# Optimization experiments

Hardware: AMD Instinct MI355X
Metric: run time of the kernel (lower is better)

## Reference

```python
import jax, jax.numpy as jnp
import numpy as np

HIDDEN = 128
INPUT_SIZE = 64
NUM_ACTIONS = 16
BATCH = 65536


def _uniform(key, shape, scale):
    return jax.random.uniform(key, shape, jnp.float32, -scale, scale)


def setup_inputs() -> dict:
    key = jax.random.key(0)
    ks = jax.random.split(key, 14)
    s = 1.0 / np.sqrt(HIDDEN)  # pytorch LSTM/Linear init scale
    return {
        "x": jax.random.normal(ks[0], (BATCH, INPUT_SIZE), jnp.float32),
        # layer 0 LSTM weights (gate order: i, f, g, o)
        "Wih0": _uniform(ks[1], (4 * HIDDEN, INPUT_SIZE), s),
        "Whh0": _uniform(ks[2], (4 * HIDDEN, HIDDEN), s),
        "bih0": _uniform(ks[3], (4 * HIDDEN,), s),
        "bhh0": _uniform(ks[4], (4 * HIDDEN,), s),
        # layer 1 LSTM weights
        "Wih1": _uniform(ks[5], (4 * HIDDEN, HIDDEN), s),
        "Whh1": _uniform(ks[6], (4 * HIDDEN, HIDDEN), s),
        "bih1": _uniform(ks[7], (4 * HIDDEN,), s),
        "bhh1": _uniform(ks[8], (4 * HIDDEN,), s),
        # policy / value heads
        "Wp": _uniform(ks[9], (NUM_ACTIONS, HIDDEN), s),
        "bp": _uniform(ks[10], (NUM_ACTIONS,), s),
        "Wv": _uniform(ks[11], (1, HIDDEN), s),
        "bv": _uniform(ks[12], (1,), s),
    }


def _lstm_cell(x, h, c, Wih, Whh, bih, bhh):
    # gates: [B, 4H], pytorch gate order i, f, g, o
    g = x @ Wih.T + bih + h @ Whh.T + bhh
    i, f, gg, o = jnp.split(g, 4, axis=-1)
    i = jax.nn.sigmoid(i)
    f = jax.nn.sigmoid(f)
    gg = jnp.tanh(gg)
    o = jax.nn.sigmoid(o)
    c2 = f * c + i * gg
    h2 = o * jnp.tanh(c2)
    return h2, c2


def reference(x, Wih0, Whh0, bih0, bhh0, Wih1, Whh1, bih1, bhh1, Wp, bp, Wv, bv):
    B = x.shape[0]
    z = jnp.zeros((B, HIDDEN), x.dtype)  # state=None -> zero init
    # seq_len == 1: single step through the 2-layer stack
    h0, c0 = _lstm_cell(x, z, z, Wih0, Whh0, bih0, bhh0)
    h1, c1 = _lstm_cell(h0, z, z, Wih1, Whh1, bih1, bhh1)
    out = h1[None]  # [1, B, H] like pytorch LSTM output
    policy = out @ Wp.T + bp  # gumbel=True -> raw logits
    value = out @ Wv.T + bv
    return policy, value
```

## Files before the change

### kernel.cpp

```cpp
#include <hip/hip_runtime.h>
#include <hip/hip_bf16.h>

#define BATCH 65536
#define IN    64
#define H     128
#define NA    16
#define NBLK  256
#define TPB   512

typedef __bf16 bf16x8 __attribute__((ext_vector_type(8)));
typedef float  f32x4  __attribute__((ext_vector_type(4)));

union Frag { uint4 u; bf16x8 v; };
struct F32x8 { float4 a, b; };

#define EXP2F(v) __builtin_amdgcn_exp2f(v)
#define RCPF(v)  __builtin_amdgcn_rcpf(v)
#define K1 1.442695041f
#define K2 2.885390082f

__device__ __forceinline__ F32x8 ld8f(const float* p) {
    F32x8 r;
    r.a = *reinterpret_cast<const float4*>(p);
    r.b = *reinterpret_cast<const float4*>(p + 4);
    return r;
}
__device__ __forceinline__ Frag cvt8(F32x8 x) {
    Frag f;
    f.v[0]=(__bf16)x.a.x; f.v[1]=(__bf16)x.a.y; f.v[2]=(__bf16)x.a.z; f.v[3]=(__bf16)x.a.w;
    f.v[4]=(__bf16)x.b.x; f.v[5]=(__bf16)x.b.y; f.v[6]=(__bf16)x.b.z; f.v[7]=(__bf16)x.b.w;
    return f;
}
__device__ __forceinline__ Frag cvt44(float4 a, float4 b) {
    Frag f;
    f.v[0]=(__bf16)a.x; f.v[1]=(__bf16)a.y; f.v[2]=(__bf16)a.z; f.v[3]=(__bf16)a.w;
    f.v[4]=(__bf16)b.x; f.v[5]=(__bf16)b.y; f.v[6]=(__bf16)b.z; f.v[7]=(__bf16)b.w;
    return f;
}
__device__ __forceinline__ unsigned pk2(float lo, float hi) {
    unsigned short l = __builtin_bit_cast(unsigned short, (__bf16)lo);
    unsigned short h = __builtin_bit_cast(unsigned short, (__bf16)hi);
    return (unsigned)l | ((unsigned)h << 16);
}
__device__ __forceinline__ float clamp30(float v) {
    return __builtin_fminf(__builtin_fmaxf(v, -30.0f), 30.0f);
}
__device__ __forceinline__ float lstm_h(float ip, float gp, float op) {
    ip = clamp30(ip); gp = clamp30(gp); op = clamp30(op);
    const float Ei = EXP2F(-K1 * ip);
    const float Eg = EXP2F( K2 * gp);
    const float c2 = (Eg - 1.0f) * RCPF((1.0f + Ei) * (Eg + 1.0f));
    const float Eo = EXP2F(-K1 * op);
    const float Ec = EXP2F( K2 * c2);
    return (Ec - 1.0f) * RCPF((1.0f + Eo) * (Ec + 1.0f));
}

__global__ __launch_bounds__(TPB, 2)
void lstm_fused(const float* __restrict__ x,
                const float* __restrict__ Wih0,
                const float* __restrict__ bih0,
                const float* __restrict__ bhh0,
                const float* __restrict__ Wih1,
                const float* __restrict__ bih1,
                const float* __restrict__ bhh1,
                const float* __restrict__ Wp,
                const float* __restrict__ bp,
                const float* __restrict__ Wv,
                const float* __restrict__ bv,
                float* __restrict__ out)
{
    __shared__ __align__(16) uint4 w0s[384 * 8];
    __shared__ __align__(16) uint4 w1s[384 * 16];
    __shared__ __align__(16) uint4 wph[32 * 16];
    __shared__ float b0s[384];
    __shared__ float b1s[384];

    const int tid  = threadIdx.x;
    const int wave = tid >> 6;
    const int lane = tid & 63;
    const int q    = lane >> 4;
    const int m    = lane & 15;
    const int rbase = blockIdx.x * 256 + wave * 32;
    const f32x4 vzero = {0.f, 0.f, 0.f, 0.f};

    F32x8 xr[2][2];
#pragma unroll
    for (int s2 = 0; s2 < 2; ++s2) {
        const float* xp = x + (size_t)(rbase + s2 * 16 + m) * IN + q * 8;
        xr[s2][0] = ld8f(xp);
        xr[s2][1] = ld8f(xp + 32);
    }
    const float4 bpr = *reinterpret_cast<const float4*>(bp + q * 4);
    const float  bvv = bv[0];

#pragma unroll
    for (int r = 0; r < 6; ++r) {
        const int idx = tid + (r << 9);
        const int j = idx >> 3, s = idx & 7;
        const int g = j >> 7, h = j & 127;
        const int srow = h + ((g == 0) ? 0 : (g + 1) * 128);
        Frag f = cvt8(ld8f(Wih0 + (size_t)srow * IN + s * 8));
        w0s[(j << 3) + (s ^ (j & 7))] = f.u;
    }
#pragma unroll
    for (int r = 0; r < 12; ++r) {
        const int idx = tid + (r << 9);
        const int j = idx >> 4, s = idx & 15;
        const int g = j >> 7, h = j & 127;
        const int srow = h + ((g == 0) ? 0 : (g + 1) * 128);
        const int kt = s >> 2, qq = s & 3;
        const float* pA = Wih1 + (size_t)srow * H + kt * 32 + qq * 4;
        Frag f = cvt44(*reinterpret_cast<const float4*>(pA),
                       *reinterpret_cast<const float4*>(pA + 16));
        w1s[(j << 4) + (s ^ (j & 7))] = f.u;
    }
    {
        const int j = tid >> 4, s = tid & 15;
        const int kt = s >> 2, qq = s & 3;
        Frag f;
        if (j <= 16) {
            const float* base = (j < 16) ? (Wp + (size_t)j * H) : Wv;
            const float* pA = base + kt * 32 + qq * 4;
            f = cvt44(*reinterpret_cast<const float4*>(pA),
                      *reinterpret_cast<const float4*>(pA + 16));
        } else {
            f.u = make_uint4(0u, 0u, 0u, 0u);
        }
        wph[(j << 4) + (s ^ (j & 7))] = f.u;
    }
#pragma unroll
    for (int r = 0; r < 2; ++r) {
        const int t = tid + (r << 9);
        if (t < 384) {
            const int g = t >> 7, h = t & 127;
            const int srow = h + ((g == 0) ? 0 : (g + 1) * 128);
            b0s[t] = bih0[srow] + bhh0[srow];
        } else if (t < 768) {
            const int tt = t - 384;
            const int g = tt >> 7, h = tt & 127;
            const int srow = h + ((g == 0) ? 0 : (g + 1) * 128);
            b1s[tt] = bih1[srow] + bhh1[srow];
        }
    }

    __syncthreads();

    const int swz = m & 7;
    Frag xb[2][2];
#pragma unroll
    for (int s2 = 0; s2 < 2; ++s2) {
        xb[s2][0] = cvt8(xr[s2][0]);
        xb[s2][1] = cvt8(xr[s2][1]);
    }

    unsigned hw0[2][16];
#pragma unroll
    for (int nc = 0; nc < 8; ++nc) {
        f32x4 acc[3][2];
#pragma unroll
        for (int g = 0; g < 3; ++g) { acc[g][0] = vzero; acc[g][1] = vzero; }
#pragma unroll
        for (int g = 0; g < 3; ++g) {
            const int n = g * 128 + nc * 16 + m;
#pragma unroll
            for (int kt = 0; kt < 2; ++kt) {
                Frag a; a.u = w0s[(n << 3) + ((kt * 4 + q) ^ swz)];
#pragma unroll
                for (int s2 = 0; s2 < 2; ++s2)
                    acc[g][s2] = __builtin_amdgcn_mfma_f32_16x16x32_bf16(
                        a.v, xb[s2][kt].v, acc[g][s2], 0, 0, 0);
            }
        }
        const f32x4 bI = *reinterpret_cast<const f32x4*>(b0s +       nc * 16 + q * 4);
        const f32x4 bG = *reinterpret_cast<const f32x4*>(b0s + 128 + nc * 16 + q * 4);
        const f32x4 bO = *reinterpret_cast<const f32x4*>(b0s + 256 + nc * 16 + q * 4);
#pragma unroll
        for (int s2 = 0; s2 < 2; ++s2)
#pragma unroll
            for (int u = 0; u < 2; ++u) {
                const float ha = lstm_h(acc[0][s2][2*u]   + bI[2*u],
                                        acc[1][s2][2*u]   + bG[2*u],
                                        acc[2][s2][2*u]   + bO[2*u]);
                const float hb = lstm_h(acc[0][s2][2*u+1] + bI[2*u+1],
                                        acc[1][s2][2*u+1] + bG[2*u+1],
                                        acc[2][s2][2*u+1] + bO[2*u+1]);
                hw0[s2][nc * 2 + u] = pk2(ha, hb);
            }
    }

    unsigned hw1[2][16];
#pragma unroll
    for (int nc = 0; nc < 8; ++nc) {
        f32x4 acc[3][2];
#pragma unroll
        for (int g = 0; g < 3; ++g) { acc[g][0] = vzero; acc[g][1] = vzero; }
#pragma unroll
        for (int kt = 0; kt < 4; ++kt) {
            Frag b[2];
#pragma unroll
            for (int s2 = 0; s2 < 2; ++s2)
                b[s2].u = make_uint4(hw0[s2][4*kt], hw0[s2][4*kt+1],
                                     hw0[s2][4*kt+2], hw0[s2][4*kt+3]);
#pragma unroll
            for (int g = 0; g < 3; ++g) {
                const int n = g * 128 + nc * 16 + m;
                Frag a; a.u = w1s[(n << 4) + ((kt * 4 + q) ^ swz)];
#pragma unroll
                for (int s2 = 0; s2 < 2; ++s2)
                    acc[g][s2] = __builtin_amdgcn_mfma_f32_16x16x32_bf16(
                        a.v, b[s2].v, acc[g][s2], 0, 0, 0);
            }
        }
        const f32x4 bI = *reinterpret_cast<const f32x4*>(b1s +       nc * 16 + q * 4);
        const f32x4 bG = *reinterpret_cast<const f32x4*>(b1s + 128 + nc * 16 + q * 4);
        const f32x4 bO = *reinterpret_cast<const f32x4*>(b1s + 256 + nc * 16 + q * 4);
#pragma unroll
        for (int s2 = 0; s2 < 2; ++s2)
#pragma unroll
            for (int u = 0; u < 2; ++u) {
                const float ha = lstm_h(acc[0][s2][2*u]   + bI[2*u],
                                        acc[1][s2][2*u]   + bG[2*u],
                                        acc[2][s2][2*u]   + bO[2*u]);
                const float hb = lstm_h(acc[0][s2][2*u+1] + bI[2*u+1],
                                        acc[1][s2][2*u+1] + bG[2*u+1],
                                        acc[2][s2][2*u+1] + bO[2*u+1]);
                hw1[s2][nc * 2 + u] = pk2(ha, hb);
            }
    }

    f32x4 ap[2], av[2];
    ap[0] = vzero; ap[1] = vzero; av[0] = vzero; av[1] = vzero;
#pragma unroll
    for (int kt = 0; kt < 4; ++kt) {
        Frag a0; a0.u = wph[( m       << 4) + ((kt * 4 + q) ^ swz)];
        Frag a1; a1.u = wph[((16 + m) << 4) + ((kt * 4 + q) ^ swz)];
#pragma unroll
        for (int s2 = 0; s2 < 2; ++s2) {
            Frag b; b.u = make_uint4(hw1[s2][4*kt], hw1[s2][4*kt+1],
                                     hw1[s2][4*kt+2], hw1[s2][4*kt+3]);
            ap[s2] = __builtin_amdgcn_mfma_f32_16x16x32_bf16(a0.v, b.v, ap[s2], 0, 0, 0);
            av[s2] = __builtin_amdgcn_mfma_f32_16x16x32_bf16(a1.v, b.v, av[s2], 0, 0, 0);
        }
    }
#pragma unroll
    for (int s2 = 0; s2 < 2; ++s2) {
        const int row = rbase + s2 * 16 + m;
        f32x4 po;
        po[0] = ap[s2][0] + bpr.x; po[1] = ap[s2][1] + bpr.y;
        po[2] = ap[s2][2] + bpr.z; po[3] = ap[s2][3] + bpr.w;
        *reinterpret_cast<f32x4*>(out + (size_t)row * NA + q * 4) = po;
        if (q == 0) out[(size_t)BATCH * NA + row] = av[s2][0] + bvv;
    }
}

extern "C" void kernel_launch(void* const* d_in, const int* in_sizes, int n_in,
                              void* d_out, int out_size, void* d_ws, size_t ws_size,
                              hipStream_t stream) {
    lstm_fused<<<dim3(NBLK), dim3(TPB), 0, stream>>>(
        (const float*)d_in[0], (const float*)d_in[1],
        (const float*)d_in[3], (const float*)d_in[4],
        (const float*)d_in[5], (const float*)d_in[7],
        (const float*)d_in[8], (const float*)d_in[9],
        (const float*)d_in[10], (const float*)d_in[11],
        (const float*)d_in[12], (float*)d_out);
}
```

Baseline: 107.3 us.

## Fuse head MFMAs into layer-1 loop and keep h0 as fragments

Stores layer-0 hidden outputs directly as packed bf16 MFMA B-fragments instead of a flat word array. It also folds the policy/value head MFMAs into the layer-1 output loop, consuming each pair of column chunks as soon as it is produced, so the full hw1 array is never held. The layer-1 loop is no longer unrolled (unroll 1). The aim is lower register pressure and better MFMA/activation interleaving, at the cost of loop overhead and less scheduling freedom across iterations.

```diff
diff --git a/kernel.cpp b/kernel.cpp
--- a/kernel.cpp
+++ b/kernel.cpp
@@ -153,7 +153,7 @@
         xb[s2][1] = cvt8(xr[s2][1]);
     }
 
-    unsigned hw0[2][16];
+    Frag b1[2][4];
 #pragma unroll
     for (int nc = 0; nc < 8; ++nc) {
         f32x4 acc[3][2];
@@ -175,73 +175,62 @@
         const f32x4 bG = *reinterpret_cast<const f32x4*>(b0s + 128 + nc * 16 + q * 4);
         const f32x4 bO = *reinterpret_cast<const f32x4*>(b0s + 256 + nc * 16 + q * 4);
 #pragma unroll
-        for (int s2 = 0; s2 < 2; ++s2)
-#pragma unroll
-            for (int u = 0; u < 2; ++u) {
-                const float ha = lstm_h(acc[0][s2][2*u]   + bI[2*u],
-                                        acc[1][s2][2*u]   + bG[2*u],
-                                        acc[2][s2][2*u]   + bO[2*u]);
-                const float hb = lstm_h(acc[0][s2][2*u+1] + bI[2*u+1],
-                                        acc[1][s2][2*u+1] + bG[2*u+1],
-                                        acc[2][s2][2*u+1] + bO[2*u+1]);
-                hw0[s2][nc * 2 + u] = pk2(ha, hb);
-            }
-    }
-
-    unsigned hw1[2][16];
-#pragma unroll
+        for (int s2 = 0; s2 < 2; ++s2) {
+            const float h0a = lstm_h(acc[0][s2][0] + bI[0], acc[1][s2][0] + bG[0], acc[2][s2][0] + bO[0]);
+            const float h0b = lstm_h(acc[0][s2][1] + bI[1], acc[1][s2][1] + bG[1], acc[2][s2][1] + bO[1]);
+            const float h1a = lstm_h(acc[0][s2][2] + bI[2], acc[1][s2][2] + bG[2], acc[2][s2][2] + bO[2]);
+            const float h1b = lstm_h(acc[0][s2][3] + bI[3], acc[1][s2][3] + bG[3], acc[2][s2][3] + bO[3]);
+            const unsigned wu0 = pk2(h0a, h0b);
+            const unsigned wu1 = pk2(h1a, h1b);
+            if ((nc & 1) == 0) { b1[s2][nc >> 1].u.x = wu0; b1[s2][nc >> 1].u.y = wu1; }
+            else               { b1[s2][nc >> 1].u.z = wu0; b1[s2][nc >> 1].u.w = wu1; }
+        }
+    }
+
+    f32x4 ap[2], av[2];
+    ap[0] = vzero; ap[1] = vzero; av[0] = vzero; av[1] = vzero;
+    uint2 hold[2];
+#pragma unroll 1
     for (int nc = 0; nc < 8; ++nc) {
         f32x4 acc[3][2];
 #pragma unroll
         for (int g = 0; g < 3; ++g) { acc[g][0] = vzero; acc[g][1] = vzero; }
+        const int nbase = nc * 16 + m;
 #pragma unroll
         for (int kt = 0; kt < 4; ++kt) {
-            Frag b[2];
-#pragma unroll
-            for (int s2 = 0; s2 < 2; ++s2)
-                b[s2].u = make_uint4(hw0[s2][4*kt], hw0[s2][4*kt+1],
-                                     hw0[s2][4*kt+2], hw0[s2][4*kt+3]);
 #pragma unroll
             for (int g = 0; g < 3; ++g) {
-                const int n = g * 128 + nc * 16 + m;
-                Frag a; a.u = w1s[(n << 4) + ((kt * 4 + q) ^ swz)];
+                Frag a; a.u = w1s[((g * 128 + nbase) << 4) + ((kt * 4 + q) ^ swz)];
 #pragma unroll
                 for (int s2 = 0; s2 < 2; ++s2)
                     acc[g][s2] = __builtin_amdgcn_mfma_f32_16x16x32_bf16(
-                        a.v, b[s2].v, acc[g][s2], 0, 0, 0);
+                        a.v, b1[s2][kt].v, acc[g][s2], 0, 0, 0);
             }
         }
         const f32x4 bI = *reinterpret_cast<const f32x4*>(b1s +       nc * 16 + q * 4);
         const f32x4 bG = *reinterpret_cast<const f32x4*>(b1s + 128 + nc * 16 + q * 4);
         const f32x4 bO = *reinterpret_cast<const f32x4*>(b1s + 256 + nc * 16 + q * 4);
 #pragma unroll
-        for (int s2 = 0; s2 < 2; ++s2)
-#pragma unroll
-            for (int u = 0; u < 2; ++u) {
-                const float ha = lstm_h(acc[0][s2][2*u]   + bI[2*u],
-                                        acc[1][s2][2*u]   + bG[2*u],
-                                        acc[2][s2][2*u]   + bO[2*u]);
-                const float hb = lstm_h(acc[0][s2][2*u+1] + bI[2*u+1],
-                                        acc[1][s2][2*u+1] + bG[2*u+1],
-                                        acc[2][s2][2*u+1] + bO[2*u+1]);
-                hw1[s2][nc * 2 + u] = pk2(ha, hb);
+        for (int s2 = 0; s2 < 2; ++s2) {
+            const float h0a = lstm_h(acc[0][s2][0] + bI[0], acc[1][s2][0] + bG[0], acc[2][s2][0] + bO[0]);
+            const float h0b = lstm_h(acc[0][s2][1] + bI[1], acc[1][s2][1] + bG[1], acc[2][s2][1] + bO[1]);
+            const float h1a = lstm_h(acc[0][s2][2] + bI[2], acc[1][s2][2] + bG[2], acc[2][s2][2] + bO[2]);
+            const float h1b = lstm_h(acc[0][s2][3] + bI[3], acc[1][s2][3] + bG[3], acc[2][s2][3] + bO[3]);
+            const unsigned wu0 = pk2(h0a, h0b);
+            const unsigned wu1 = pk2(h1a, h1b);
+            if ((nc & 1) == 0) {
+                hold[s2].x = wu0; hold[s2].y = wu1;
+            } else {
+                Frag bh; bh.u = make_uint4(hold[s2].x, hold[s2].y, wu0, wu1);
+                const int ktp = nc >> 1;
+                Frag a0; a0.u = wph[( m       << 4) + ((ktp * 4 + q) ^ swz)];
+                Frag a1; a1.u = wph[((16 + m) << 4) + ((ktp * 4 + q) ^ swz)];
+                ap[s2] = __builtin_amdgcn_mfma_f32_16x16x32_bf16(a0.v, bh.v, ap[s2], 0, 0, 0);
+                av[s2] = __builtin_amdgcn_mfma_f32_16x16x32_bf16(a1.v, bh.v, av[s2], 0, 0, 0);
             }
-    }
-
-    f32x4 ap[2], av[2];
-    ap[0] = vzero; ap[1] = vzero; av[0] = vzero; av[1] = vzero;
-#pragma unroll
-    for (int kt = 0; kt < 4; ++kt) {
-        Frag a0; a0.u = wph[( m       << 4) + ((kt * 4 + q) ^ swz)];
-        Frag a1; a1.u = wph[((16 + m) << 4) + ((kt * 4 + q) ^ swz)];
-#pragma unroll
-        for (int s2 = 0; s2 < 2; ++s2) {
-            Frag b; b.u = make_uint4(hw1[s2][4*kt], hw1[s2][4*kt+1],
-                                     hw1[s2][4*kt+2], hw1[s2][4*kt+3]);
-            ap[s2] = __builtin_amdgcn_mfma_f32_16x16x32_bf16(a0.v, b.v, ap[s2], 0, 0, 0);
-            av[s2] = __builtin_amdgcn_mfma_f32_16x16x32_bf16(a1.v, b.v, av[s2], 0, 0, 0);
-        }
-    }
+        }
+    }
+
 #pragma unroll
     for (int s2 = 0; s2 < 2; ++s2) {
         const int row = rbase + s2 * 16 + m;
```

Measured after the change: 109.8 us. +2.4%, slower.

## Precompute bf16 swizzled weights and biases in a prep kernel

Applied to the files above, without the earlier changes.

Moves the fp32-to-bf16 conversion, gate reordering, swizzling and bias summation of all weights out of the main kernel into a small prep kernel that writes a packed image to workspace. Each main-kernel block then copies that image into shared memory with plain 16-byte loads, instead of redoing the conversion in all 256 blocks. This adds a second kernel launch and a global round trip through workspace. The per-block weight load also becomes half the bytes.

```diff
diff --git a/kernel.cpp b/kernel.cpp
--- a/kernel.cpp
+++ b/kernel.cpp
@@ -7,6 +7,14 @@
 #define NA    16
 #define NBLK  256
 #define TPB   512
+
+#define NW0   3072
+#define NW1   6144
+#define NPH   512
+#define OW1   3072
+#define OPH   9216
+#define OBIAS 9728
+#define NTOT  9920
 
 typedef __bf16 bf16x8 __attribute__((ext_vector_type(8)));
 typedef float  f32x4  __attribute__((ext_vector_type(4)));
@@ -55,67 +63,40 @@
     return (Ec - 1.0f) * RCPF((1.0f + Eo) * (Ec + 1.0f));
 }
 
-__global__ __launch_bounds__(TPB, 2)
-void lstm_fused(const float* __restrict__ x,
-                const float* __restrict__ Wih0,
-                const float* __restrict__ bih0,
-                const float* __restrict__ bhh0,
-                const float* __restrict__ Wih1,
-                const float* __restrict__ bih1,
-                const float* __restrict__ bhh1,
-                const float* __restrict__ Wp,
-                const float* __restrict__ bp,
-                const float* __restrict__ Wv,
-                const float* __restrict__ bv,
-                float* __restrict__ out)
+__device__ __forceinline__ int igo_row(int j) {
+    const int g = j >> 7, h = j & 127;
+    return h + ((g == 0) ? 0 : (g + 1) * 128);
+}
+
+__global__ __launch_bounds__(256)
+void lstm_prep(const float* __restrict__ Wih0,
+               const float* __restrict__ bih0,
+               const float* __restrict__ bhh0,
+               const float* __restrict__ Wih1,
+               const float* __restrict__ bih1,
+               const float* __restrict__ bhh1,
+               const float* __restrict__ Wp,
+               const float* __restrict__ Wv,
+               uint4* __restrict__ ws)
 {
-    __shared__ __align__(16) uint4 w0s[384 * 8];
-    __shared__ __align__(16) uint4 w1s[384 * 16];
-    __shared__ __align__(16) uint4 wph[32 * 16];
-    __shared__ float b0s[384];
-    __shared__ float b1s[384];
-
-    const int tid  = threadIdx.x;
-    const int wave = tid >> 6;
-    const int lane = tid & 63;
-    const int q    = lane >> 4;
-    const int m    = lane & 15;
-    const int rbase = blockIdx.x * 256 + wave * 32;
-    const f32x4 vzero = {0.f, 0.f, 0.f, 0.f};
-
-    F32x8 xr[2][2];
-#pragma unroll
-    for (int s2 = 0; s2 < 2; ++s2) {
-        const float* xp = x + (size_t)(rbase + s2 * 16 + m) * IN + q * 8;
-        xr[s2][0] = ld8f(xp);
-        xr[s2][1] = ld8f(xp + 32);
-    }
-    const float4 bpr = *reinterpret_cast<const float4*>(bp + q * 4);
-    const float  bvv = bv[0];
-
-#pragma unroll
-    for (int r = 0; r < 6; ++r) {
-        const int idx = tid + (r << 9);
-        const int j = idx >> 3, s = idx & 7;
-        const int g = j >> 7, h = j & 127;
-        const int srow = h + ((g == 0) ? 0 : (g + 1) * 128);
+    const int G = blockIdx.x * 256 + threadIdx.x;
+    if (G < NW0) {
+        const int j = G >> 3, s = G & 7;
+        const int srow = igo_row(j);
         Frag f = cvt8(ld8f(Wih0 + (size_t)srow * IN + s * 8));
-        w0s[(j << 3) + (s ^ (j & 7))] = f.u;
-    }
-#pragma unroll
-    for (int r = 0; r < 12; ++r) {
-        const int idx = tid + (r << 9);
-        const int j = idx >> 4, s = idx & 15;
-        const int g = j >> 7, h = j & 127;
-        const int srow = h + ((g == 0) ? 0 : (g + 1) * 128);
+        ws[(j << 3) + (s ^ (j & 7))] = f.u;
+    } else if (G < OPH) {
+        const int t = G - OW1;
+        const int j = t >> 4, s = t & 15;
+        const int srow = igo_row(j);
         const int kt = s >> 2, qq = s & 3;
         const float* pA = Wih1 + (size_t)srow * H + kt * 32 + qq * 4;
         Frag f = cvt44(*reinterpret_cast<const float4*>(pA),
                        *reinterpret_cast<const float4*>(pA + 16));
-        w1s[(j << 4) + (s ^ (j & 7))] = f.u;
-    }
-    {
-        const int j = tid >> 4, s = tid & 15;
+        ws[OW1 + (j << 4) + (s ^ (j & 7))] = f.u;
+    } else if (G < OBIAS) {
+        const int t = G - OPH;
+        const int j = t >> 4, s = t & 15;
         const int kt = s >> 2, qq = s & 3;
         Frag f;
         if (j <= 16) {
@@ -126,24 +107,59 @@
         } else {
             f.u = make_uint4(0u, 0u, 0u, 0u);
         }
-        wph[(j << 4) + (s ^ (j & 7))] = f.u;
-    }
-#pragma unroll
-    for (int r = 0; r < 2; ++r) {
-        const int t = tid + (r << 9);
-        if (t < 384) {
-            const int g = t >> 7, h = t & 127;
-            const int srow = h + ((g == 0) ? 0 : (g + 1) * 128);
-            b0s[t] = bih0[srow] + bhh0[srow];
-        } else if (t < 768) {
-            const int tt = t - 384;
-            const int g = tt >> 7, h = tt & 127;
-            const int srow = h + ((g == 0) ? 0 : (g + 1) * 128);
-            b1s[tt] = bih1[srow] + bhh1[srow];
-        }
-    }
+        ws[OPH + (j << 4) + (s ^ (j & 7))] = f.u;
+    } else if (G < NTOT) {
+        const int fbase = (G - OBIAS) * 4;
+        float4 r;
+#pragma unroll
+        for (int e = 0; e < 4; ++e) {
+            const int i = fbase + e;
+            float v;
+            if (i < 384) { const int sr = igo_row(i);        v = bih0[sr] + bhh0[sr]; }
+            else         { const int sr = igo_row(i - 384);  v = bih1[sr] + bhh1[sr]; }
+            reinterpret_cast<float*>(&r)[e] = v;
+        }
+        ws[G] = __builtin_bit_cast(uint4, r);
+    }
+}
+
+__global__ __launch_bounds__(TPB, 2)
+void lstm_fused(const float* __restrict__ x,
+                const uint4* __restrict__ ws,
+                const float* __restrict__ bp,
+                const float* __restrict__ bv,
+                float* __restrict__ out)
+{
+    __shared__ __align__(16) uint4 smem[NTOT];
+
+    const int tid  = threadIdx.x;
+    const int wave = tid >> 6;
+    const int lane = tid & 63;
+    const int q    = lane >> 4;
+    const int m    = lane & 15;
+    const int rbase = blockIdx.x * 256 + wave * 32;
+    const f32x4 vzero = {0.f, 0.f, 0.f, 0.f};
+
+    F32x8 xr[2][2];
+#pragma unroll
+    for (int s2 = 0; s2 < 2; ++s2) {
+        const float* xp = x + (size_t)(rbase + s2 * 16 + m) * IN + q * 8;
+        xr[s2][0] = ld8f(xp);
+        xr[s2][1] = ld8f(xp + 32);
+    }
+    const float4 bpr = *reinterpret_cast<const float4*>(bp + q * 4);
+    const float  bvv = bv[0];
+
+#pragma unroll
+    for (int i = tid; i < NTOT; i += TPB) smem[i] = ws[i];
 
     __syncthreads();
+
+    const uint4* w0s = smem;
+    const uint4* w1s = smem + OW1;
+    const uint4* wph = smem + OPH;
+    const float* b0s = reinterpret_cast<const float*>(smem + OBIAS);
+    const float* b1s = b0s + 384;
 
     const int swz = m & 7;
     Frag xb[2][2];
@@ -256,11 +272,12 @@
 extern "C" void kernel_launch(void* const* d_in, const int* in_sizes, int n_in,
                               void* d_out, int out_size, void* d_ws, size_t ws_size,
                               hipStream_t stream) {
+    uint4* ws = (uint4*)d_ws;
+    lstm_prep<<<dim3((NTOT + 255) / 256), dim3(256), 0, stream>>>(
+        (const float*)d_in[1], (const float*)d_in[3], (const float*)d_in[4],
+        (const float*)d_in[5], (const float*)d_in[7], (const float*)d_in[8],
+        (const float*)d_in[9], (const float*)d_in[11], ws);
     lstm_fused<<<dim3(NBLK), dim3(TPB), 0, stream>>>(
-        (const float*)d_in[0], (const float*)d_in[1],
-        (const float*)d_in[3], (const float*)d_in[4],
-        (const float*)d_in[5], (const float*)d_in[7],
-        (const float*)d_in[8], (const float*)d_in[9],
-        (const float*)d_in[10], (const float*)d_in[11],
-        (const float*)d_in[12], (float*)d_out);
-}
+        (const float*)d_in[0], ws,
+        (const float*)d_in[10], (const float*)d_in[12], (float*)d_out);
+}
```

Result: slower. 110.4 us (+2.9%).
